# Kernel tuning notes

Measured on AMD Instinct MI355X. Metric: run time of the kernel, lower is better.

The kernel has to match this reference:

```python
import jax, jax.numpy as jnp
import numpy as np

N1, E1, D_IN, D_OUT = 100000, 1600000, 128, 128
N2, E2, NB = 1024, 200000, 30


def setup_inputs() -> dict:
    key = jax.random.key(0)
    ks = jax.random.split(key, 11)
    return {
        "x_g1": jax.random.normal(ks[0], (N1, D_IN), jnp.float32),
        "W_stc": jax.random.normal(ks[1], (D_IN, D_OUT), jnp.float32) / np.sqrt(D_IN),
        "b_stc": jax.random.normal(ks[2], (D_OUT,), jnp.float32) * 0.01,
        "x_g2": jax.random.normal(ks[3], (N2, N2), jnp.float32),
        "basis": jax.random.normal(ks[4], (NB, N2, N2), jnp.float32) / np.sqrt(N2 * NB),
        "att": jax.random.normal(ks[5], (E2, NB), jnp.float32),
        "root": jax.random.normal(ks[6], (N2, N2), jnp.float32) / np.sqrt(N2),
        "bias_rgcn": jax.random.normal(ks[7], (N2,), jnp.float32) * 0.01,
        "edge_index_g1": jax.random.randint(ks[8], (2, E1), 0, N1, jnp.int64),
        "edge_index_g2": jax.random.randint(ks[9], (2, E2), 0, N2, jnp.int64),
        "edge_type_g2": jax.random.randint(ks[10], (E2,), 0, E2, jnp.int64),
    }


def reference(x_g1, W_stc, b_stc, x_g2, basis, att, root, bias_rgcn,
              edge_index_g1, edge_index_g2, edge_type_g2):
    # ---- STCConv on G1: mean-aggregate neighbor features, then linear ----
    src1, dst1 = edge_index_g1[0], edge_index_g1[1]
    deg1 = jax.ops.segment_sum(jnp.ones((E1,), x_g1.dtype), dst1, num_segments=N1)
    agg1 = jax.ops.segment_sum(x_g1[src1], dst1, num_segments=N1)  # [N1, D_IN]
    agg1 = agg1 / jnp.maximum(deg1, 1.0)[:, None]
    h1 = jax.nn.relu(agg1 @ W_stc + b_stc)
    out1 = jax.nn.log_softmax(h1, axis=1)

    # ---- RGCNConv on G2 with basis decomposition: W_r = sum_b att[r,b] B_b ----
    src2, dst2 = edge_index_g2[0], edge_index_g2[1]
    deg2 = jnp.maximum(
        jax.ops.segment_sum(jnp.ones((E2,), x_g2.dtype), dst2, num_segments=N2), 1.0)
    x_src = x_g2[src2]            # [E2, N2] gathered source features
    coeff = att[edge_type_g2]     # [E2, NB] per-edge basis coefficients
    h2 = x_g2 @ root + bias_rgcn  # root/self transform
    # aggregate per basis first (cheap [N2,N2] matmul after scatter)
    for b in range(NB):
        S = jax.ops.segment_sum(x_src * coeff[:, b:b + 1], dst2, num_segments=N2)
        h2 = h2 + (S / deg2[:, None]) @ basis[b]
    h2 = jax.nn.relu(h2)
    out2 = jax.nn.log_softmax(h2, axis=1)
    return (out1, out2)
```

## Files before the change

### kernel.cpp

```cpp
#include <hip/hip_runtime.h>

typedef unsigned short u16;
typedef unsigned int u32;
typedef unsigned long long u64;
typedef __attribute__((ext_vector_type(8))) short short8;
typedef __attribute__((ext_vector_type(4))) float floatx4;

#define NBMAX 2048

__device__ __forceinline__ float b2f(u16 u) {
    u32 x = ((u32)u) << 16; float f; __builtin_memcpy(&f, &x, 4); return f;
}
__device__ __forceinline__ u16 f2b(float f) {
    u32 x; __builtin_memcpy(&x, &f, 4);
    u32 r = (x + 0x7fffu + ((x >> 16) & 1u)) >> 16;
    return (u16)r;
}
__device__ __forceinline__ float ldf(const void* p, long i, int isf) {
    return isf ? ((const float*)p)[i] : b2f(((const u16*)p)[i]);
}
__device__ __forceinline__ void stf(void* p, long i, float v, int isf) {
    if (isf) ((float*)p)[i] = v; else ((u16*)p)[i] = f2b(v);
}
__device__ __forceinline__ int ldidx(const int* w, long i, int is64) {
    return is64 ? w[2 * i] : w[i];
}
__device__ __forceinline__ void gload16(const u16* g, u16* l) {
    __builtin_amdgcn_global_load_lds((const __attribute__((address_space(1))) void*)g,
                                     (__attribute__((address_space(3))) void*)l, 16, 0, 0);
}

__global__ void detect_kernel(const u32* __restrict__ xw, const u32* __restrict__ iw,
                              int* __restrict__ flags) {
    int lane = threadIdx.x;
    u32 w = xw[lane];
    u32 b1 = (w >> 8) & 0x7f;
    int isbf = (b1 >= 0x38 && b1 <= 0x41) ? 1 : 0;
    int cbf = __popcll(__ballot(isbf));
    u32 hi = iw[2 * lane + 1];
    int cz = __popcll(__ballot(hi == 0u));
    if (lane == 0) {
        flags[0] = (cbf < 32) ? 1 : 0;
        flags[1] = (cz >= 56) ? 1 : 0;
    }
}


__global__ __launch_bounds__(256)
void bcount_kernel(const int* __restrict__ eiw, int E, int chunk,
                   int* __restrict__ bcnt, int NB, int shift,
                   const int* __restrict__ flags) {
    __shared__ int h[NBMAX];
    int t = threadIdx.x;
    for (int i = t; i < NB; i += 256) h[i] = 0;
    __syncthreads();
    int is64 = flags[1];
    int lo = blockIdx.x * chunk;
    int hi = lo + chunk; if (hi > E) hi = E;
    for (int e = lo + t; e < hi; e += 256)
        atomicAdd(&h[ldidx(eiw, (long)E + e, is64) >> shift], 1);
    __syncthreads();
    for (int i = t; i < NB; i += 256)
        if (h[i]) atomicAdd(&bcnt[i], h[i]);
}

__global__ void bscan_kernel(const int* __restrict__ bcnt, int* __restrict__ boff,
                             int* __restrict__ bcur, int NB) {
    __shared__ int sm[1024];
    int t = threadIdx.x;
    int a = (2 * t < NB) ? bcnt[2 * t] : 0;
    int b = (2 * t + 1 < NB) ? bcnt[2 * t + 1] : 0;
    int s = a + b;
    sm[t] = s;
    __syncthreads();
    for (int o = 1; o < 1024; o <<= 1) {
        int x = (t >= o) ? sm[t - o] : 0;
        __syncthreads();
        sm[t] += x;
        __syncthreads();
    }
    int ex = sm[t] - s;
    if (2 * t < NB) { boff[2 * t] = ex; bcur[2 * t] = ex; }
    if (2 * t + 1 < NB) { boff[2 * t + 1] = ex + a; bcur[2 * t + 1] = ex + a; }
    if (t == 1023) boff[NB] = sm[1023];
}

__global__ __launch_bounds__(256)
void bscatter_kernel(const int* __restrict__ eiw, int E, int chunk,
                     int* __restrict__ bcur, int NB, u32* __restrict__ pair,
                     const int* __restrict__ flags) {
    __shared__ int h[NBMAX];
    __shared__ int cur[NBMAX];
    int t = threadIdx.x;
    for (int i = t; i < NB; i += 256) h[i] = 0;
    __syncthreads();
    int is64 = flags[1];
    int lo = blockIdx.x * chunk;
    int hi = lo + chunk; if (hi > E) hi = E;
    for (int e = lo + t; e < hi; e += 256)
        atomicAdd(&h[ldidx(eiw, (long)E + e, is64) >> 7], 1);
    __syncthreads();
    for (int i = t; i < NB; i += 256) {
        int c = h[i];
        h[i] = c ? atomicAdd(&bcur[i], c) : 0;
        cur[i] = 0;
    }
    __syncthreads();
    for (int e = lo + t; e < hi; e += 256) {
        int src = ldidx(eiw, e, is64);
        int d = ldidx(eiw, (long)E + e, is64);
        int b = d >> 7;
        int p = atomicAdd(&cur[b], 1);
        pair[h[b] + p] = ((u32)(d & 127) << 25) | (u32)src;
    }
}

__global__ __launch_bounds__(256)
void bscatter2_kernel(const int* __restrict__ ei, const int* __restrict__ et, int E,
                      int chunk, int* __restrict__ bcur, u32* __restrict__ elist2,
                      const int* __restrict__ flags) {
    __shared__ int h[1024];
    __shared__ int cur[1024];
    int t = threadIdx.x;
    for (int i = t; i < 1024; i += 256) h[i] = 0;
    __syncthreads();
    int is64 = flags[1];
    int lo = blockIdx.x * chunk;
    int hi = lo + chunk; if (hi > E) hi = E;
    for (int e = lo + t; e < hi; e += 256)
        atomicAdd(&h[ldidx(ei, (long)E + e, is64)], 1);
    __syncthreads();
    for (int i = t; i < 1024; i += 256) {
        int c = h[i];
        h[i] = c ? atomicAdd(&bcur[i], c) : 0;
        cur[i] = 0;
    }
    __syncthreads();
    for (int e = lo + t; e < hi; e += 256) {
        int s = ldidx(ei, e, is64);
        int d = ldidx(ei, (long)E + e, is64);
        int ty = ldidx(et, e, is64);
        int p = atomicAdd(&cur[d], 1);
        elist2[h[d] + p] = (u32)s | ((u32)ty << 10);
    }
}

__global__ __launch_bounds__(256)
void bucketfill2_kernel(const u32* __restrict__ pair, const int* __restrict__ boff,
                        int NB, int N1, int* __restrict__ off1, int* __restrict__ elist) {
    __shared__ int cnt[128], pre[128], soff[128], cur[128];
    int b = blockIdx.x, t = threadIdx.x;
    int lo = boff[b], hi = boff[b + 1];
    if (t < 128) cnt[t] = 0;
    __syncthreads();
    for (int i = lo + t; i < hi; i += 256)
        atomicAdd(&cnt[pair[i] >> 25], 1);
    __syncthreads();
    if (t < 128) pre[t] = cnt[t];
    __syncthreads();
    for (int o = 1; o < 128; o <<= 1) {
        int x = (t >= o && t < 128) ? pre[t - o] : 0;
        __syncthreads();
        if (t < 128) pre[t] += x;
        __syncthreads();
    }
    int d0 = b << 7;
    if (t < 128) {
        int s = lo + pre[t] - cnt[t];
        soff[t] = s;
        cur[t] = 0;
        if (d0 + t < N1) off1[d0 + t] = s;
    }
    if (b == NB - 1 && t == 0) off1[N1] = hi;
    __syncthreads();
    for (int i = lo + t; i < hi; i += 256) {
        u32 v = pair[i];
        int dl = v >> 25;
        int p = atomicAdd(&cur[dl], 1);
        elist[soff[dl] + p] = (int)(v & 0x1FFFFFFu);
    }
}

__global__ void count_kernel(const int* __restrict__ eiw, int E, int* __restrict__ cnt,
                             const int* __restrict__ flags) {
    int e = blockIdx.x * 256 + threadIdx.x;
    if (e < E) atomicAdd(&cnt[ldidx(eiw, (long)E + e, flags[1])], 1);
}

__global__ void scan_block_kernel(const int* __restrict__ in, int* __restrict__ out,
                                  int* __restrict__ bsum, int n) {
    __shared__ int sm[1024];
    int t = threadIdx.x;
    int i = blockIdx.x * 1024 + t;
    int v = (i < n) ? in[i] : 0;
    sm[t] = v;
    __syncthreads();
    for (int o = 1; o < 1024; o <<= 1) {
        int x = (t >= o) ? sm[t - o] : 0;
        __syncthreads();
        sm[t] += x;
        __syncthreads();
    }
    if (i < n) out[i] = sm[t] - v;
    if (t == 1023) bsum[blockIdx.x] = sm[1023];
}

__global__ void scan_small_kernel(int* __restrict__ bsum, int nb) {
    __shared__ int sm[128];
    int t = threadIdx.x;
    int v = (t < nb) ? bsum[t] : 0;
    sm[t] = v;
    __syncthreads();
    for (int o = 1; o < 128; o <<= 1) {
        int x = (t >= o) ? sm[t - o] : 0;
        __syncthreads();
        sm[t] += x;
        __syncthreads();
    }
    if (t < nb) bsum[t] = sm[t] - v;
}

__global__ void scan_add_kernel(int* __restrict__ off, const int* __restrict__ bsum,
                                int n, int total) {
    int i = blockIdx.x * 1024 + threadIdx.x;
    if (i < n) off[i] += bsum[blockIdx.x];
    if (i == 0) off[n] = total;
}

__global__ void fill_kernel(const int* __restrict__ eiw, int E, const int* __restrict__ off,
                            int* __restrict__ cur, int* __restrict__ elist,
                            const int* __restrict__ flags) {
    int e = blockIdx.x * 256 + threadIdx.x;
    if (e < E) {
        int is64 = flags[1];
        int d = ldidx(eiw, (long)E + e, is64);
        int p = atomicAdd(&cur[d], 1);
        elist[off[d] + p] = ldidx(eiw, e, is64);
    }
}

__global__ void cvt4_kernel(const void* __restrict__ in, u64* __restrict__ out, long n4,
                            const int* __restrict__ flags) {
    long i = (long)blockIdx.x * 256 + threadIdx.x;
    if (i >= n4) return;
    if (flags[0]) {
        float4 v = ((const float4*)in)[i];
        out[i] = (u64)f2b(v.x) | ((u64)f2b(v.y) << 16) | ((u64)f2b(v.z) << 32) |
                 ((u64)f2b(v.w) << 48);
    } else {
        out[i] = ((const u64*)in)[i];
    }
}

__global__ void agg_kernel(const void* __restrict__ xraw, const u32* __restrict__ xb,
                           const int* __restrict__ off, const int* __restrict__ elist,
                           u32* __restrict__ aggbf, int N, const int* __restrict__ flags,
                           int useXB) {
    int node = blockIdx.x * 4 + (threadIdx.x >> 6);
    if (node >= N) return;
    int lane = threadIdx.x & 63;
    int b = off[node], e = off[node + 1];
    float a0 = 0.f, a1 = 0.f, c0 = 0.f, c1 = 0.f;
    if (useXB) {
        int i = b;
        for (; i + 4 <= e; i += 4) {
            int s0 = elist[i], s1 = elist[i + 1], s2 = elist[i + 2], s3 = elist[i + 3];
            u32 v0 = xb[(long)s0 * 64 + lane];
            u32 v1 = xb[(long)s1 * 64 + lane];
            u32 v2 = xb[(long)s2 * 64 + lane];
            u32 v3 = xb[(long)s3 * 64 + lane];
            a0 += b2f((u16)(v0 & 0xffffu)) + b2f((u16)(v2 & 0xffffu));
            a1 += b2f((u16)(v0 >> 16)) + b2f((u16)(v2 >> 16));
            c0 += b2f((u16)(v1 & 0xffffu)) + b2f((u16)(v3 & 0xffffu));
            c1 += b2f((u16)(v1 >> 16)) + b2f((u16)(v3 >> 16));
        }
        for (; i < e; i++) {
            u32 v = xb[(long)elist[i] * 64 + lane];
            a0 += b2f((u16)(v & 0xffffu));
            a1 += b2f((u16)(v >> 16));
        }
        a0 += c0; a1 += c1;
    } else if (flags[0]) {
        const float* xf = (const float*)xraw;
        for (int i = b; i < e; i++) {
            long s = elist[i];
            a0 += xf[s * 128 + 2 * lane];
            a1 += xf[s * 128 + 2 * lane + 1];
        }
    } else {
        const u32* xu = (const u32*)xraw;
        for (int i = b; i < e; i++) {
            u32 v = xu[(long)elist[i] * 64 + lane];
            a0 += b2f((u16)(v & 0xffffu));
            a1 += b2f((u16)(v >> 16));
        }
    }
    int dg = e - b; if (dg < 1) dg = 1;
    float inv = 1.0f / (float)dg;
    aggbf[(long)node * 64 + lane] = (u32)f2b(a0 * inv) | ((u32)f2b(a1 * inv) << 16);
}

__global__ void transpose_kernel(const void* __restrict__ in, long inOff,
                                 u16* __restrict__ out, int R, int C,
                                 const int* __restrict__ flags) {
    __shared__ u16 tile[32][33];
    int isf = flags[0];
    int tx = threadIdx.x, ty = threadIdx.y;
    int x = blockIdx.x * 32 + tx;
#pragma unroll
    for (int i = 0; i < 4; i++) {
        int y = blockIdx.y * 32 + ty + i * 8;
        long idx = inOff + (long)y * C + x;
        tile[ty + i * 8][tx] = isf ? f2b(((const float*)in)[idx]) : ((const u16*)in)[idx];
    }
    __syncthreads();
    int x2 = blockIdx.y * 32 + tx;
#pragma unroll
    for (int i = 0; i < 4; i++) {
        int y2 = blockIdx.x * 32 + ty + i * 8;
        out[(long)y2 * R + x2] = tile[tx][ty + i * 8];
    }
}

__global__ __launch_bounds__(256)
void scatterA_lds_kernel(const u32* __restrict__ elist, const int* __restrict__ off,
                         const void* __restrict__ att, u16* __restrict__ Abf,
                         int b0, int CH, const int* __restrict__ flags) {
    __shared__ float sA[15 * 1024];
    const int d = blockIdx.x, t = threadIdx.x;
    const int b = off[d], e = off[d + 1];
    int cnt = e - b; if (cnt < 1) cnt = 1;
    const float inv = 1.0f / (float)cnt;
    const int tot = CH << 10;
    for (int i = t; i < tot; i += 256) sA[i] = 0.f;
    __syncthreads();
    const int isf = flags[0];
    for (int i = b + t; i < e; i += 256) {
        u32 v = elist[i];
        int s = v & 1023;
        long tb = (long)(v >> 10) * 30 + b0;
        for (int bb = 0; bb < CH; bb++)
            atomicAdd(&sA[(bb << 10) + s], ldf(att, tb + bb, isf) * inv);
    }
    __syncthreads();
    const long obase = (long)d * 256 + t;
    for (int bb = 0; bb < CH; bb++) {
        int base = (bb << 10) + (t << 2);
        u64 p = (u64)f2b(sA[base]) | ((u64)f2b(sA[base + 1]) << 16) |
                ((u64)f2b(sA[base + 2]) << 32) | ((u64)f2b(sA[base + 3]) << 48);
        ((u64*)Abf)[(long)bb * 262144 + obase] = p;
    }
}

__global__ __launch_bounds__(256)
void gemm_stc(const u16* __restrict__ A, const u16* __restrict__ BT,
              void* __restrict__ Cb, const void* __restrict__ bias,
              const int* __restrict__ flags, int M) {
    __shared__ u16 Bs[4][4096];
    __shared__ float sred[2][2][128];
    const int t = threadIdx.x;
    const int isf = flags[0];
    const int row0 = blockIdx.x * 128;
    const int lane = t & 63, wave = t >> 6;
    const int wrow = (wave >> 1) * 64, wcol = (wave & 1) * 64;
    const int quad = lane >> 4, l16 = lane & 15;

#pragma unroll
    for (int kt = 0; kt < 4; kt++) {
#pragma unroll
        for (int h = 0; h < 2; h++) {
            int r2 = h * 64 + wave * 16 + (lane >> 2);
            int clog = (lane & 3) ^ ((r2 >> 1) & 3);
            gload16(BT + (long)r2 * 128 + kt * 32 + clog * 8,
                    &Bs[kt][(h * 64 + wave * 16) * 32]);
        }
    }
    u32 aoff[4];
#pragma unroll
    for (int i = 0; i < 4; i++) {
        int ga = row0 + wrow + i * 16 + l16; if (ga >= M) ga = M - 1;
        aoff[i] = (u32)ga * 128u + (u32)(quad * 8);
    }
    int bidx[4];
#pragma unroll
    for (int j = 0; j < 4; j++) {
        int rb = wcol + j * 16 + l16;
        bidx[j] = rb * 32 + ((quad ^ ((rb >> 1) & 3)) * 8);
    }
    floatx4 acc[4][4];
#pragma unroll
    for (int i = 0; i < 4; i++)
#pragma unroll
        for (int j = 0; j < 4; j++)
            acc[i][j] = (floatx4){0.f, 0.f, 0.f, 0.f};
    __syncthreads();

#pragma unroll
    for (int kt = 0; kt < 4; kt++) {
        short8 af[4], bfr[4];
#pragma unroll
        for (int i = 0; i < 4; i++)
            af[i] = *(const short8*)(A + aoff[i] + kt * 32);
#pragma unroll
        for (int j = 0; j < 4; j++)
            bfr[j] = *(const short8*)&Bs[kt][bidx[j]];
#pragma unroll
        for (int i = 0; i < 4; i++)
#pragma unroll
            for (int j = 0; j < 4; j++)
                acc[i][j] = __builtin_amdgcn_mfma_f32_16x16x32_bf16(af[i], bfr[j], acc[i][j], 0, 0, 0);
    }

    const int colhalf = wave & 1;
    float bv[4];
#pragma unroll
    for (int j = 0; j < 4; j++)
        bv[j] = ldf(bias, wcol + j * 16 + l16, isf);
    float Mp[4][4];
#pragma unroll
    for (int i = 0; i < 4; i++)
#pragma unroll
        for (int rr = 0; rr < 4; rr++) {
            float m = 0.f;
#pragma unroll
            for (int j = 0; j < 4; j++) {
                float v = fmaxf(acc[i][j][rr] + bv[j], 0.f);
                acc[i][j][rr] = v;
                m = fmaxf(m, v);
            }
#pragma unroll
            for (int o = 1; o < 16; o <<= 1) m = fmaxf(m, __shfl_xor(m, o, 64));
            if (l16 == 0) sred[0][colhalf][wrow + i * 16 + quad * 4 + rr] = m;
        }
    __syncthreads();
#pragma unroll
    for (int i = 0; i < 4; i++)
#pragma unroll
        for (int rr = 0; rr < 4; rr++) {
            int r2 = wrow + i * 16 + quad * 4 + rr;
            Mp[i][rr] = fmaxf(sred[0][0][r2], sred[0][1][r2]);
            float s = 0.f;
#pragma unroll
            for (int j = 0; j < 4; j++) s += __expf(acc[i][j][rr] - Mp[i][rr]);
#pragma unroll
            for (int o = 1; o < 16; o <<= 1) s += __shfl_xor(s, o, 64);
            if (l16 == 0) sred[1][colhalf][r2] = s;
        }
    __syncthreads();
#pragma unroll
    for (int i = 0; i < 4; i++)
#pragma unroll
        for (int rr = 0; rr < 4; rr++) {
            int r2 = wrow + i * 16 + quad * 4 + rr;
            long crow = (long)row0 + r2;
            if (crow < M) {
                float lg = __logf(sred[1][0][r2] + sred[1][1][r2]);
#pragma unroll
                for (int j = 0; j < 4; j++)
                    stf(Cb, crow * 128 + wcol + j * 16 + l16,
                        acc[i][j][rr] - Mp[i][rr] - lg, isf);
            }
        }
}

template <int MODE>
__global__ __launch_bounds__(256)
void gemm_bt(const u16* __restrict__ A, long aBatch,
             const u16* __restrict__ BT,
             float* __restrict__ Cf, void* __restrict__ Cb,
             const void* __restrict__ bias, const int* __restrict__ flags,
             int M, int lda, int ldb, int ldc,
             int colOffDim, long cBatch, int kSplitStride, int kLen) {
    __shared__ u16 As[4096];
    __shared__ u16 Bs[4096];
    const int t = threadIdx.x;
    const int gx = gridDim.x, gy = gridDim.y;
    const int nwg = gx * gy * gridDim.z;
    const int bid = blockIdx.x + gx * (blockIdx.y + gy * blockIdx.z);
    const int q = nwg >> 3, r = nwg & 7;
    const int xcd = bid & 7, idx = bid >> 3;
    const int nbid = (xcd < r ? xcd * (q + 1) : r * (q + 1) + (xcd - r) * q) + idx;
    const int bx = nbid % gx;
    const int by = (nbid / gx) % gy;
    const int bz = nbid / (gx * gy);

    const int isf = flags[0];
    A += (long)bz * aBatch;
    const int kBase = bz * kSplitStride;
    const int row0 = bx * 128;
    const int n0 = by * 128;
    const int lane = t & 63, wave = t >> 6;
    const int wrow = (wave >> 1) * 64, wcol = (wave & 1) * 64;
    const int quad = lane >> 4, l16 = lane & 15;

    long aoff[2], boff[2];
    u16 *ldsA[2], *ldsB[2];
#pragma unroll
    for (int h = 0; h < 2; h++) {
        int r2 = h * 64 + wave * 16 + (lane >> 2);
        int clog = (lane & 3) ^ ((r2 >> 1) & 3);
        int ga = row0 + r2; if (ga >= M) ga = M - 1;
        aoff[h] = (long)ga * lda + clog * 8;
        boff[h] = (long)(n0 + r2) * ldb + clog * 8;
        ldsA[h] = &As[(h * 64 + wave * 16) * 32];
        ldsB[h] = &Bs[(h * 64 + wave * 16) * 32];
    }
    int aidx[4], bidx[4];
#pragma unroll
    for (int i = 0; i < 4; i++) {
        int ra = wrow + i * 16 + l16;
        aidx[i] = ra * 32 + ((quad ^ ((ra >> 1) & 3)) * 8);
        int rb = wcol + i * 16 + l16;
        bidx[i] = rb * 32 + ((quad ^ ((rb >> 1) & 3)) * 8);
    }

    floatx4 acc[4][4];
#pragma unroll
    for (int i = 0; i < 4; i++)
#pragma unroll
        for (int j = 0; j < 4; j++)
            acc[i][j] = (floatx4){0.f, 0.f, 0.f, 0.f};

    for (int kt = kBase; kt < kBase + kLen; kt += 32) {
        __syncthreads();
#pragma unroll
        for (int h = 0; h < 2; h++) {
            gload16(A + aoff[h] + kt, ldsA[h]);
            gload16(BT + boff[h] + kt, ldsB[h]);
        }
        __syncthreads();
        short8 af[4], bfr[4];
#pragma unroll
        for (int i = 0; i < 4; i++) {
            af[i]  = *(const short8*)&As[aidx[i]];
            bfr[i] = *(const short8*)&Bs[bidx[i]];
        }
#pragma unroll
        for (int i = 0; i < 4; i++)
#pragma unroll
            for (int j = 0; j < 4; j++)
                acc[i][j] = __builtin_amdgcn_mfma_f32_16x16x32_bf16(af[i], bfr[j], acc[i][j], 0, 0, 0);
    }

    const long colOff = (long)bz * colOffDim;
    float* Cfp = Cf ? Cf + (long)bz * cBatch : nullptr;
#pragma unroll
    for (int i = 0; i < 4; i++)
#pragma unroll
        for (int j = 0; j < 4; j++)
#pragma unroll
            for (int r2 = 0; r2 < 4; r2++) {
                long crow = row0 + wrow + i * 16 + quad * 4 + r2;
                long ccol = n0 + wcol + j * 16 + l16;
                float v = acc[i][j][r2];
                if (MODE == 1) {
                    ((u16*)Cb)[crow * ldc + colOff + ccol] = f2b(v);
                } else if (MODE == 2) {
                    Cfp[crow * ldc + ccol] = v + ldf(bias, ccol, isf);
                } else if (MODE == 3) {
                    Cfp[crow * ldc + ccol] += v;
                } else {
                    Cfp[crow * ldc + ccol] = v;
                }
            }
}

__global__ void softmax2_kernel(const float* __restrict__ Zr, const float* __restrict__ Zp,
                                void* __restrict__ out, long outOff, int nsplit,
                                const int* __restrict__ flags) {
    int row = blockIdx.x;
    int t = threadIdx.x;
    __shared__ float red[4];
    float4 v = ((const float4*)Zr)[(long)row * 256 + t];
    for (int s = 0; s < nsplit; s++) {
        float4 p = ((const float4*)Zp)[(long)s * 262144 + (long)row * 256 + t];
        v.x += p.x; v.y += p.y; v.z += p.z; v.w += p.w;
    }
    float z[4] = {fmaxf(v.x, 0.f), fmaxf(v.y, 0.f), fmaxf(v.z, 0.f), fmaxf(v.w, 0.f)};
    float m = fmaxf(fmaxf(z[0], z[1]), fmaxf(z[2], z[3]));
#pragma unroll
    for (int o = 1; o < 64; o <<= 1) m = fmaxf(m, __shfl_xor(m, o, 64));
    int wave = t >> 6, lane = t & 63;
    if (lane == 0) red[wave] = m;
    __syncthreads();
    m = fmaxf(fmaxf(red[0], red[1]), fmaxf(red[2], red[3]));
    __syncthreads();
    float s4 = __expf(z[0] - m) + __expf(z[1] - m) + __expf(z[2] - m) + __expf(z[3] - m);
#pragma unroll
    for (int o = 1; o < 64; o <<= 1) s4 += __shfl_xor(s4, o, 64);
    if (lane == 0) red[wave] = s4;
    __syncthreads();
    float lg = __logf(red[0] + red[1] + red[2] + red[3]);
    long base = outOff + (long)row * 1024 + t * 4;
    if (flags[0]) {
        float4 o = {z[0] - m - lg, z[1] - m - lg, z[2] - m - lg, z[3] - m - lg};
        ((float4*)out)[base >> 2] = o;
    } else {
        u64 p = (u64)f2b(z[0] - m - lg) | ((u64)f2b(z[1] - m - lg) << 16) |
                ((u64)f2b(z[2] - m - lg) << 32) | ((u64)f2b(z[3] - m - lg) << 48);
        ((u64*)out)[base >> 2] = p;
    }
}


extern "C" void kernel_launch(void* const* d_in, const int* in_sizes, int n_in,
                              void* d_out, int out_size, void* d_ws, size_t ws_size,
                              hipStream_t stream) {
    const void* x_g1 = d_in[0];
    const void* W    = d_in[1];
    const void* bstc = d_in[2];
    const void* x_g2 = d_in[3];
    const void* basis= d_in[4];
    const void* att  = d_in[5];
    const void* root = d_in[6];
    const void* brg  = d_in[7];
    const int* ei1   = (const int*)d_in[8];
    const int* ei2   = (const int*)d_in[9];
    const int* et2   = (const int*)d_in[10];
    const int N1 = in_sizes[0] / 128;
    const int E1 = in_sizes[8] / 2;
    const int E2 = in_sizes[9] / 2;

    const size_t MB = 1ull << 20;
    const int cCH[7] = {15, 10, 6, 5, 3, 2, 1};
    const int cNS[7] = { 8,  8, 8, 8, 8, 4, 2};
    int CH = 1, NS = 1, USE_XB = 1;
    bool found = false;
    for (int pass = 0; pass < 2 && !found; pass++) {
        size_t floorP1 = pass == 0 ? 68 * MB : 42 * MB;
        for (int c = 0; c < 7; c++) {
            size_t chunk = (size_t)cCH[c] * 6 * MB;
            size_t scratch = chunk > floorP1 ? chunk : floorP1;
            size_t need = 11 * MB + (size_t)cNS[c] * 4 * MB + scratch;
            if (need <= ws_size) {
                CH = cCH[c]; NS = cNS[c]; USE_XB = (pass == 0); found = true; break;
            }
        }
    }
    if (!found) { CH = 1; NS = 1; USE_XB = 0; }
    const int NC = 30 / CH;
    const int kSp = CH * 1024 / NS;

    char* ws = (char*)d_ws;
    u16*   XT    = (u16*)(ws + 0);
    u16*   rootT = (u16*)(ws + 2 * MB);
    u16*   Xbf   = (u16*)(ws + 4 * MB);
    u16*   WT    = (u16*)(ws + 6 * MB);
    int*   deg2  = (int*)(ws + 6 * MB + 65536);
    int*   off2  = (int*)(ws + 6 * MB + 73728);
    int*   cur2  = (int*)(ws + 6 * MB + 81920);
    int*   flags = (int*)(ws + 6 * MB + 98304);
    u32*   elist2= (u32*)(ws + 6 * MB + 131072);
    float* Zr    = (float*)(ws + 7 * MB);
    float* Zp    = (float*)(ws + 11 * MB);
    char*  S     = ws + 11 * MB + (size_t)NS * 4 * MB;
    int* off1   = (int*)(S);
    int* bktCnt = (int*)(S + 512 * 1024);
    int* bktOff = (int*)(S + 544 * 1024);
    int* bktCur = (int*)(S + 576 * 1024);
    int* bsum   = (int*)(S + 608 * 1024);
    int* deg1f  = (int*)(S + 1 * MB);
    int* cur1f  = (int*)(S + 1536 * 1024);
    u32* pair1  = (u32*)(S + 2 * MB);
    int* elist  = (int*)(S + 9 * MB);
    u16* xg1b   = (u16*)(S + 16 * MB);
    u16* aggbf  = (u16*)(S + (USE_XB ? 42 * MB : 16 * MB));
    u16*   Abf   = (u16*)S;
    u16*   ST    = (u16*)(S + (size_t)CH * 2 * MB);
    u16*   basTc = (u16*)(S + (size_t)CH * 4 * MB);

    detect_kernel<<<1, 64, 0, stream>>>((const u32*)x_g1, (const u32*)ei1, flags);

    hipMemsetAsync(deg2, 0, 4096, stream);

    const int NB1 = (N1 + 127) >> 7;
    if (NB1 <= NBMAX) {
        hipMemsetAsync(bktCnt, 0, (size_t)(NB1 + 1) * 4, stream);
        const int chunk = 8192;
        const int nbk = (E1 + chunk - 1) / chunk;
        bcount_kernel<<<nbk, 256, 0, stream>>>(ei1, E1, chunk, bktCnt, NB1, 7, flags);
        bscan_kernel<<<1, 1024, 0, stream>>>(bktCnt, bktOff, bktCur, NB1);
        bscatter_kernel<<<nbk, 256, 0, stream>>>(ei1, E1, chunk, bktCur, NB1, pair1, flags);
        bucketfill2_kernel<<<NB1, 256, 0, stream>>>(pair1, bktOff, NB1, N1, off1, elist);
    } else {
        hipMemsetAsync(deg1f, 0, 1048576, stream);
        count_kernel<<<(E1 + 255) / 256, 256, 0, stream>>>(ei1, E1, deg1f, flags);
        int nb1 = (N1 + 1023) / 1024;
        scan_block_kernel<<<nb1, 1024, 0, stream>>>(deg1f, off1, bsum, N1);
        scan_small_kernel<<<1, 128, 0, stream>>>(bsum, nb1);
        scan_add_kernel<<<nb1, 1024, 0, stream>>>(off1, bsum, N1, E1);
        fill_kernel<<<(E1 + 255) / 256, 256, 0, stream>>>(ei1, E1, off1, cur1f, elist, flags);
    }
    if (USE_XB) {
        long n4 = (long)N1 * 32;
        cvt4_kernel<<<(int)((n4 + 255) / 256), 256, 0, stream>>>(x_g1, (u64*)xg1b, n4, flags);
    }
    agg_kernel<<<(N1 + 3) / 4, 256, 0, stream>>>(x_g1, (const u32*)xg1b, off1, elist,
                                                 (u32*)aggbf, N1, flags, USE_XB);
    transpose_kernel<<<dim3(4, 4), dim3(32, 8), 0, stream>>>(W, 0, WT, 128, 128, flags);
    gemm_stc<<<dim3((N1 + 127) / 128), 256, 0, stream>>>(aggbf, WT, d_out, bstc, flags, N1);

    const int chunk2 = 8192;
    const int nbk2 = (E2 + chunk2 - 1) / chunk2;
    bcount_kernel<<<nbk2, 256, 0, stream>>>(ei2, E2, chunk2, deg2, 1024, 0, flags);
    bscan_kernel<<<1, 1024, 0, stream>>>(deg2, off2, cur2, 1024);
    bscatter2_kernel<<<nbk2, 256, 0, stream>>>(ei2, et2, E2, chunk2, cur2, elist2, flags);
    cvt4_kernel<<<1024, 256, 0, stream>>>(x_g2, (u64*)Xbf, 262144, flags);
    transpose_kernel<<<dim3(32, 32), dim3(32, 8), 0, stream>>>(x_g2, 0, XT, 1024, 1024, flags);
    transpose_kernel<<<dim3(32, 32), dim3(32, 8), 0, stream>>>(root, 0, rootT, 1024, 1024, flags);
    gemm_bt<2><<<dim3(8, 8, 1), 256, 0, stream>>>(
        Xbf, 0, rootT, Zr, nullptr, brg, flags, 1024, 1024, 1024, 1024, 0, 0, 0, 1024);

    for (int c = 0; c < NC; c++) {
        scatterA_lds_kernel<<<1024, 256, 0, stream>>>(elist2, off2, att, Abf,
                                                      c * CH, CH, flags);
        transpose_kernel<<<dim3(32, CH * 32), dim3(32, 8), 0, stream>>>(
            basis, (long)c * CH * 1048576, basTc, CH * 1024, 1024, flags);
        gemm_bt<1><<<dim3(8, 8, CH), 256, 0, stream>>>(
            Abf, 1048576, XT, nullptr, ST, nullptr, flags,
            1024, 1024, 1024, CH * 1024, 1024, 0, 0, 1024);
        if (c == 0) {
            gemm_bt<4><<<dim3(8, 8, NS), 256, 0, stream>>>(
                ST, 0, basTc, Zp, nullptr, nullptr, flags,
                1024, CH * 1024, CH * 1024, 1024, 0, 1048576, kSp, kSp);
        } else {
            gemm_bt<3><<<dim3(8, 8, NS), 256, 0, stream>>>(
                ST, 0, basTc, Zp, nullptr, nullptr, flags,
                1024, CH * 1024, CH * 1024, 1024, 0, 1048576, kSp, kSp);
        }
    }
    softmax2_kernel<<<1024, 256, 0, stream>>>(Zr, Zp, d_out, (long)N1 * 128, NS, flags);
}
```

Baseline: 832.3 us.

## Double GEMM K-tile to 64 and split-K the root GEMM

The bf16 MFMA GEMM now stages 64-wide K tiles (16 KB of LDS per operand) with an 8-way XOR swizzle. This halves the number of barrier pairs per K sweep and issues more loads per sync. The root transform GEMM is split four ways along K into separate partial buffers, giving it 256 workgroups instead of 64. Its bias add moves into the final softmax kernel, which sums the four partials. This costs extra workspace and partial-sum traffic, and the larger LDS footprint may lower occupancy.

```diff
diff --git a/kernel.cpp b/kernel.cpp
--- a/kernel.cpp
+++ b/kernel.cpp
@@ -468,11 +468,11 @@
 void gemm_bt(const u16* __restrict__ A, long aBatch,
              const u16* __restrict__ BT,
              float* __restrict__ Cf, void* __restrict__ Cb,
-             const void* __restrict__ bias, const int* __restrict__ flags,
+             const int* __restrict__ flags,
              int M, int lda, int ldb, int ldc,
              int colOffDim, long cBatch, int kSplitStride, int kLen) {
-    __shared__ u16 As[4096];
-    __shared__ u16 Bs[4096];
+    __shared__ u16 As[8192];
+    __shared__ u16 Bs[8192];
     const int t = threadIdx.x;
     const int gx = gridDim.x, gy = gridDim.y;
     const int nwg = gx * gy * gridDim.z;
@@ -484,7 +484,6 @@
     const int by = (nbid / gx) % gy;
     const int bz = nbid / (gx * gy);
 
-    const int isf = flags[0];
     A += (long)bz * aBatch;
     const int kBase = bz * kSplitStride;
     const int row0 = bx * 128;
@@ -493,25 +492,28 @@
     const int wrow = (wave >> 1) * 64, wcol = (wave & 1) * 64;
     const int quad = lane >> 4, l16 = lane & 15;
 
-    long aoff[2], boff[2];
-    u16 *ldsA[2], *ldsB[2];
-#pragma unroll
-    for (int h = 0; h < 2; h++) {
-        int r2 = h * 64 + wave * 16 + (lane >> 2);
-        int clog = (lane & 3) ^ ((r2 >> 1) & 3);
+    long aoff[4], boff[4];
+    u16 *ldsA[4], *ldsB[4];
+#pragma unroll
+    for (int h = 0; h < 4; h++) {
+        int r2 = h * 32 + wave * 8 + (lane >> 3);
+        int clog = (lane & 7) ^ ((r2 >> 1) & 7);
         int ga = row0 + r2; if (ga >= M) ga = M - 1;
         aoff[h] = (long)ga * lda + clog * 8;
         boff[h] = (long)(n0 + r2) * ldb + clog * 8;
-        ldsA[h] = &As[(h * 64 + wave * 16) * 32];
-        ldsB[h] = &Bs[(h * 64 + wave * 16) * 32];
-    }
-    int aidx[4], bidx[4];
+        ldsA[h] = &As[(h * 32 + wave * 8) * 64];
+        ldsB[h] = &Bs[(h * 32 + wave * 8) * 64];
+    }
+    int aidx[2][4], bidx[2][4];
 #pragma unroll
     for (int i = 0; i < 4; i++) {
         int ra = wrow + i * 16 + l16;
-        aidx[i] = ra * 32 + ((quad ^ ((ra >> 1) & 3)) * 8);
         int rb = wcol + i * 16 + l16;
-        bidx[i] = rb * 32 + ((quad ^ ((rb >> 1) & 3)) * 8);
+#pragma unroll
+        for (int kk = 0; kk < 2; kk++) {
+            aidx[kk][i] = ra * 64 + (((kk * 4 + quad) ^ ((ra >> 1) & 7)) * 8);
+            bidx[kk][i] = rb * 64 + (((kk * 4 + quad) ^ ((rb >> 1) & 7)) * 8);
+        }
     }
 
     floatx4 acc[4][4];
@@ -521,25 +523,28 @@
         for (int j = 0; j < 4; j++)
             acc[i][j] = (floatx4){0.f, 0.f, 0.f, 0.f};
 
-    for (int kt = kBase; kt < kBase + kLen; kt += 32) {
-        __syncthreads();
-#pragma unroll
-        for (int h = 0; h < 2; h++) {
+    for (int kt = kBase; kt < kBase + kLen; kt += 64) {
+        __syncthreads();
+#pragma unroll
+        for (int h = 0; h < 4; h++) {
             gload16(A + aoff[h] + kt, ldsA[h]);
             gload16(BT + boff[h] + kt, ldsB[h]);
         }
         __syncthreads();
-        short8 af[4], bfr[4];
-#pragma unroll
-        for (int i = 0; i < 4; i++) {
-            af[i]  = *(const short8*)&As[aidx[i]];
-            bfr[i] = *(const short8*)&Bs[bidx[i]];
-        }
-#pragma unroll
-        for (int i = 0; i < 4; i++)
-#pragma unroll
-            for (int j = 0; j < 4; j++)
-                acc[i][j] = __builtin_amdgcn_mfma_f32_16x16x32_bf16(af[i], bfr[j], acc[i][j], 0, 0, 0);
+#pragma unroll
+        for (int kk = 0; kk < 2; kk++) {
+            short8 af[4], bfr[4];
+#pragma unroll
+            for (int i = 0; i < 4; i++) {
+                af[i]  = *(const short8*)&As[aidx[kk][i]];
+                bfr[i] = *(const short8*)&Bs[bidx[kk][i]];
+            }
+#pragma unroll
+            for (int i = 0; i < 4; i++)
+#pragma unroll
+                for (int j = 0; j < 4; j++)
+                    acc[i][j] = __builtin_amdgcn_mfma_f32_16x16x32_bf16(af[i], bfr[j], acc[i][j], 0, 0, 0);
+        }
     }
 
     const long colOff = (long)bz * colOffDim;
@@ -555,8 +560,6 @@
                 float v = acc[i][j][r2];
                 if (MODE == 1) {
                     ((u16*)Cb)[crow * ldc + colOff + ccol] = f2b(v);
-                } else if (MODE == 2) {
-                    Cfp[crow * ldc + ccol] = v + ldf(bias, ccol, isf);
                 } else if (MODE == 3) {
                     Cfp[crow * ldc + ccol] += v;
                 } else {
@@ -565,13 +568,22 @@
             }
 }
 
-__global__ void softmax2_kernel(const float* __restrict__ Zr, const float* __restrict__ Zp,
-                                void* __restrict__ out, long outOff, int nsplit,
-                                const int* __restrict__ flags) {
+__global__ void softmax2_kernel(const float* __restrict__ Zr4, const float* __restrict__ Zp,
+                                const void* __restrict__ brg, void* __restrict__ out,
+                                long outOff, int nsplit, const int* __restrict__ flags) {
     int row = blockIdx.x;
     int t = threadIdx.x;
     __shared__ float red[4];
-    float4 v = ((const float4*)Zr)[(long)row * 256 + t];
+    int isf = flags[0];
+    float4 v;
+    v.x = ldf(brg, t * 4 + 0, isf);
+    v.y = ldf(brg, t * 4 + 1, isf);
+    v.z = ldf(brg, t * 4 + 2, isf);
+    v.w = ldf(brg, t * 4 + 3, isf);
+    for (int s = 0; s < 4; s++) {
+        float4 p = ((const float4*)Zr4)[(long)s * 262144 + (long)row * 256 + t];
+        v.x += p.x; v.y += p.y; v.z += p.z; v.w += p.w;
+    }
     for (int s = 0; s < nsplit; s++) {
         float4 p = ((const float4*)Zp)[(long)s * 262144 + (long)row * 256 + t];
         v.x += p.x; v.y += p.y; v.z += p.z; v.w += p.w;
@@ -592,7 +604,7 @@
     __syncthreads();
     float lg = __logf(red[0] + red[1] + red[2] + red[3]);
     long base = outOff + (long)row * 1024 + t * 4;
-    if (flags[0]) {
+    if (isf) {
         float4 o = {z[0] - m - lg, z[1] - m - lg, z[2] - m - lg, z[3] - m - lg};
         ((float4*)out)[base >> 2] = o;
     } else {
@@ -631,7 +643,7 @@
         for (int c = 0; c < 7; c++) {
             size_t chunk = (size_t)cCH[c] * 6 * MB;
             size_t scratch = chunk > floorP1 ? chunk : floorP1;
-            size_t need = 11 * MB + (size_t)cNS[c] * 4 * MB + scratch;
+            size_t need = 23 * MB + (size_t)cNS[c] * 4 * MB + scratch;
             if (need <= ws_size) {
                 CH = cCH[c]; NS = cNS[c]; USE_XB = (pass == 0); found = true; break;
             }
@@ -651,9 +663,9 @@
     int*   cur2  = (int*)(ws + 6 * MB + 81920);
     int*   flags = (int*)(ws + 6 * MB + 98304);
     u32*   elist2= (u32*)(ws + 6 * MB + 131072);
-    float* Zr    = (float*)(ws + 7 * MB);
-    float* Zp    = (float*)(ws + 11 * MB);
-    char*  S     = ws + 11 * MB + (size_t)NS * 4 * MB;
+    float* Zp    = (float*)(ws + 7 * MB);
+    float* Zr4   = (float*)(ws + 7 * MB + (size_t)NS * 4 * MB);
+    char*  S     = ws + 23 * MB + (size_t)NS * 4 * MB;
     int* off1   = (int*)(S);
     int* bktCnt = (int*)(S + 512 * 1024);
     int* bktOff = (int*)(S + 544 * 1024);
@@ -708,8 +720,8 @@
     cvt4_kernel<<<1024, 256, 0, stream>>>(x_g2, (u64*)Xbf, 262144, flags);
     transpose_kernel<<<dim3(32, 32), dim3(32, 8), 0, stream>>>(x_g2, 0, XT, 1024, 1024, flags);
     transpose_kernel<<<dim3(32, 32), dim3(32, 8), 0, stream>>>(root, 0, rootT, 1024, 1024, flags);
-    gemm_bt<2><<<dim3(8, 8, 1), 256, 0, stream>>>(
-        Xbf, 0, rootT, Zr, nullptr, brg, flags, 1024, 1024, 1024, 1024, 0, 0, 0, 1024);
+    gemm_bt<4><<<dim3(8, 8, 4), 256, 0, stream>>>(
+        Xbf, 0, rootT, Zr4, nullptr, flags, 1024, 1024, 1024, 1024, 0, 1048576, 256, 256);
 
     for (int c = 0; c < NC; c++) {
         scatterA_lds_kernel<<<1024, 256, 0, stream>>>(elist2, off2, att, Abf,
@@ -717,17 +729,17 @@
         transpose_kernel<<<dim3(32, CH * 32), dim3(32, 8), 0, stream>>>(
             basis, (long)c * CH * 1048576, basTc, CH * 1024, 1024, flags);
         gemm_bt<1><<<dim3(8, 8, CH), 256, 0, stream>>>(
-            Abf, 1048576, XT, nullptr, ST, nullptr, flags,
+            Abf, 1048576, XT, nullptr, ST, flags,
             1024, 1024, 1024, CH * 1024, 1024, 0, 0, 1024);
         if (c == 0) {
             gemm_bt<4><<<dim3(8, 8, NS), 256, 0, stream>>>(
-                ST, 0, basTc, Zp, nullptr, nullptr, flags,
+                ST, 0, basTc, Zp, nullptr, flags,
                 1024, CH * 1024, CH * 1024, 1024, 0, 1048576, kSp, kSp);
         } else {
             gemm_bt<3><<<dim3(8, 8, NS), 256, 0, stream>>>(
-                ST, 0, basTc, Zp, nullptr, nullptr, flags,
+                ST, 0, basTc, Zp, nullptr, flags,
                 1024, CH * 1024, CH * 1024, 1024, 0, 1048576, kSp, kSp);
         }
     }
-    softmax2_kernel<<<1024, 256, 0, stream>>>(Zr, Zp, d_out, (long)N1 * 128, NS, flags);
-}
+    softmax2_kernel<<<1024, 256, 0, stream>>>(Zr4, Zp, brg, d_out, (long)N1 * 128, NS, flags);
+}
```

New measurement: 772.1 us. 7.2% less time.
